# Kernel tuning notes

Hardware: AMD Instinct MI355X
Metric: run time of the kernel (lower is better)

## Reference

```python
import jax, jax.numpy as jnp
import numpy as np

B, L, D, DIN, A, V, R = 1024, 100, 256, 704, 128, 32000, 129


def setup_inputs() -> dict:
    key = jax.random.key(0)
    ks = jax.random.split(key, 18)
    s = 0.05
    inp = {
        "x": jax.random.normal(ks[0], (B, DIN), jnp.float32),
        "h0": jax.random.normal(ks[1], (B, D), jnp.float32),
        "c0": jax.random.normal(ks[2], (B, D), jnp.float32),
        "src_enc": jax.random.normal(ks[3], (B, L, D), jnp.float32),
        "src_token_ids": jax.random.randint(ks[4], (B, L), 0, V),
        "W_ih": jax.random.normal(ks[5], (4 * D, DIN), jnp.float32) * s,
        "b_ih": jax.random.normal(ks[6], (4 * D,), jnp.float32) * s,
        "W_hh": jax.random.normal(ks[7], (4 * D, D), jnp.float32) * s,
        "b_hh": jax.random.normal(ks[8], (4 * D,), jnp.float32) * s,
        "W_attn": jax.random.normal(ks[9], (D, D), jnp.float32) * s,
        "W_att_vec": jax.random.normal(ks[10], (A * 2, 2 * D), jnp.float32) * s,
        "W_ptr": jax.random.normal(ks[11], (D, D), jnp.float32) * s,
        "rule_emb": jax.random.normal(ks[12], (R, 128), jnp.float32) * s,
        "W_rule_proj": jax.random.normal(ks[13], (D, 128), jnp.float32) * s,
        "prim_emb": jax.random.normal(ks[14], (V, 128), jnp.float32) * s,
        "W_prim_proj": jax.random.normal(ks[15], (D, 128), jnp.float32) * s,
        "w_gen": jax.random.normal(ks[16], (2, D), jnp.float32) * s,
        "b_gen": jax.random.normal(ks[17], (2,), jnp.float32) * s,
    }
    # W_att_vec maps concat(h, ctx) [2D] -> ATT (=256); keep shape (256, 512)
    inp["W_att_vec"] = inp["W_att_vec"][:256]
    return inp


def reference(x, h0, c0, src_enc, src_token_ids, W_ih, b_ih, W_hh, b_hh,
              W_attn, W_att_vec, W_ptr, rule_emb, W_rule_proj,
              prim_emb, W_prim_proj, w_gen, b_gen):
    # --- LSTMCell (torch gate order i, f, g, o) ---
    gates = x @ W_ih.T + b_ih + h0 @ W_hh.T + b_hh          # [B, 4D]
    i, f, g, o = jnp.split(gates, 4, axis=-1)
    i, f, o = jax.nn.sigmoid(i), jax.nn.sigmoid(f), jax.nn.sigmoid(o)
    c = f * c0 + i * jnp.tanh(g)
    h = o * jnp.tanh(c)                                      # [B, D]

    # --- dot-product attention over source encodings ---
    enc_proj = src_enc @ W_attn.T                            # [B, L, D]
    scores = jnp.einsum('bd,bld->bl', h, enc_proj)
    alpha = jax.nn.softmax(scores, axis=-1)
    ctx = jnp.einsum('bl,bld->bd', alpha, src_enc)
    att = jnp.tanh(jnp.concatenate([h, ctx], axis=-1) @ W_att_vec.T)  # [B, 256]

    # --- apply-rule (production) readout ---
    rule_proj = rule_emb @ W_rule_proj.T                     # [R, 256]
    log_p_rule = jax.nn.log_softmax(att @ rule_proj.T, axis=-1)  # [B, R]

    # --- primitive generation readout ---
    prim_proj = prim_emb @ W_prim_proj.T                     # [V, 256]
    p_gen_prim = jax.nn.softmax(att @ prim_proj.T, axis=-1)  # [B, V]

    # --- pointer network copy distribution over source positions ---
    ptr_scores = jnp.einsum('bld,bd->bl', src_enc @ W_ptr.T, att)
    copy_p = jax.nn.softmax(ptr_scores, axis=-1)             # [B, L]

    # --- gen vs copy gate (softmax over 2, per usage in parse()) ---
    gate = jax.nn.softmax(att @ w_gen.T + b_gen, axis=-1)    # [B, 2]

    # --- combined primitive distribution: gen + scattered copy mass ---
    p_prim = gate[:, :1] * p_gen_prim                        # [B, V]
    copy_mass = gate[:, 1:] * copy_p                         # [B, L]
    bidx = jnp.arange(p_prim.shape[0])[:, None]
    p_prim = p_prim.at[bidx, src_token_ids].add(copy_mass)
    return log_p_rule, p_prim, h, c, att
```

## Files before the change

### kernel.cpp

```cpp
#include <hip/hip_runtime.h>
#include <hip/hip_bf16.h>
#include <math.h>

#define NB   1024
#define LL   100
#define DD   256
#define DINN 704
#define VV   32000
#define RR   129
#define KAV  512
#define ROWU 129

typedef float f32x4 __attribute__((ext_vector_type(4)));
typedef float f32x2 __attribute__((ext_vector_type(2)));
typedef short s16x8 __attribute__((ext_vector_type(8)));
typedef unsigned short u16;
typedef unsigned int u32;

__device__ __forceinline__ float sigf(float x) { return 1.0f / (1.0f + __expf(-x)); }

__device__ __forceinline__ u16 f2bf(float f) {
    u32 u = __float_as_uint(f);
    u += 0x7fffu + ((u >> 16) & 1u);
    return (u16)(u >> 16);
}
__device__ __forceinline__ float bf2f(u16 s) {
    return __uint_as_float(((u32)s) << 16);
}

__global__ __launch_bounds__(256) void k_conv(
    const float* __restrict__ prim_emb, u16* __restrict__ prim_bf,
    const float* __restrict__ W_ih, u16* __restrict__ wih_bf,
    const float* __restrict__ W_hh, u16* __restrict__ whh_bf,
    const float* __restrict__ x, u16* __restrict__ x_bf,
    const float* __restrict__ h0, u16* __restrict__ h0_bf,
    const float* __restrict__ rule_emb, const float* __restrict__ W_rule_proj,
    float* __restrict__ rpT)
{
    __shared__ float re_s[128];
    const int bx = blockIdx.x, t = threadIdx.x;

    const float* src; u16* dst; int off;
    if (bx < 2000)      { src = prim_emb; dst = prim_bf; off = bx * 2048; }
    else if (bx < 2352) { src = W_ih;  dst = wih_bf; off = (bx - 2000) * 2048; }
    else if (bx < 2480) { src = W_hh;  dst = whh_bf; off = (bx - 2352) * 2048; }
    else if (bx < 2832) { src = x;     dst = x_bf;   off = (bx - 2480) * 2048; }
    else                { src = h0;    dst = h0_bf;  off = (bx - 2832) * 2048; }

    if (bx < RR && t < 128) re_s[t] = rule_emb[bx * 128 + t];

    int i = off + t * 8;
    f32x4 a = *reinterpret_cast<const f32x4*>(&src[i]);
    f32x4 b = *reinterpret_cast<const f32x4*>(&src[i + 4]);
    s16x8 r;
    r[0] = (short)f2bf(a[0]); r[1] = (short)f2bf(a[1]);
    r[2] = (short)f2bf(a[2]); r[3] = (short)f2bf(a[3]);
    r[4] = (short)f2bf(b[0]); r[5] = (short)f2bf(b[1]);
    r[6] = (short)f2bf(b[2]); r[7] = (short)f2bf(b[3]);
    *reinterpret_cast<s16x8*>(&dst[i]) = r;

    if (bx < RR) {
        __syncthreads();
        float acc = 0.f;
        const float* __restrict__ wr = &W_rule_proj[t * 128];
#pragma unroll 8
        for (int k = 0; k < 128; k += 4) {
            f32x4 w4 = *reinterpret_cast<const f32x4*>(&wr[k]);
            acc += w4[0] * re_s[k] + w4[1] * re_s[k + 1]
                 + w4[2] * re_s[k + 2] + w4[3] * re_s[k + 3];
        }
        rpT[t * 192 + bx] = acc;
    }
}

__global__ __launch_bounds__(256) void k_lstm(
    const u16* __restrict__ x_bf, const u16* __restrict__ h0_bf,
    const float* __restrict__ c0,
    const u16* __restrict__ wih_bf, const u16* __restrict__ whh_bf,
    const float* __restrict__ b_ih, const float* __restrict__ b_hh,
    float* __restrict__ out_h, float* __restrict__ out_c)
{
    const int t = threadIdx.x;
    const int lane = t & 63, w = t >> 6;
    const int lm = lane & 15, lq = lane >> 4;
    const int dg = blockIdx.x;
    const int row0 = blockIdx.y * 128 + w * 32;
    f32x4 acc[4][2] = {};

    for (int kt = 0; kt < 22; ++kt) {
        const int ko = kt * 32 + lq * 8;
        s16x8 bfr[4], afr[2];
#pragma unroll
        for (int mg = 0; mg < 4; ++mg)
            bfr[mg] = *reinterpret_cast<const s16x8*>(
                &wih_bf[(mg * 256 + dg * 16 + lm) * DINN + ko]);
#pragma unroll
        for (int ng = 0; ng < 2; ++ng)
            afr[ng] = *reinterpret_cast<const s16x8*>(
                &x_bf[(row0 + ng * 16 + lm) * DINN + ko]);
#pragma unroll
        for (int mg = 0; mg < 4; ++mg)
#pragma unroll
            for (int ng = 0; ng < 2; ++ng)
                acc[mg][ng] = __builtin_amdgcn_mfma_f32_16x16x32_bf16(
                    bfr[mg], afr[ng], acc[mg][ng], 0, 0, 0);
    }
    for (int kt = 0; kt < 8; ++kt) {
        const int ko = kt * 32 + lq * 8;
        s16x8 bfr[4], afr[2];
#pragma unroll
        for (int mg = 0; mg < 4; ++mg)
            bfr[mg] = *reinterpret_cast<const s16x8*>(
                &whh_bf[(mg * 256 + dg * 16 + lm) * DD + ko]);
#pragma unroll
        for (int ng = 0; ng < 2; ++ng)
            afr[ng] = *reinterpret_cast<const s16x8*>(
                &h0_bf[(row0 + ng * 16 + lm) * DD + ko]);
#pragma unroll
        for (int mg = 0; mg < 4; ++mg)
#pragma unroll
            for (int ng = 0; ng < 2; ++ng)
                acc[mg][ng] = __builtin_amdgcn_mfma_f32_16x16x32_bf16(
                    bfr[mg], afr[ng], acc[mg][ng], 0, 0, 0);
    }

    const int dc = dg * 16 + lq * 4;
    f32x4 bi[4];
#pragma unroll
    for (int mg = 0; mg < 4; ++mg) {
        f32x4 a4 = *reinterpret_cast<const f32x4*>(&b_ih[mg * 256 + dc]);
        f32x4 b4 = *reinterpret_cast<const f32x4*>(&b_hh[mg * 256 + dc]);
        bi[mg][0] = a4[0] + b4[0]; bi[mg][1] = a4[1] + b4[1];
        bi[mg][2] = a4[2] + b4[2]; bi[mg][3] = a4[3] + b4[3];
    }
#pragma unroll
    for (int ng = 0; ng < 2; ++ng) {
        const int row = row0 + ng * 16 + lm;
        f32x4 c4 = *reinterpret_cast<const f32x4*>(&c0[row * DD + dc]);
        f32x4 h4, cc4;
#pragma unroll
        for (int r = 0; r < 4; ++r) {
            float iv = acc[0][ng][r] + bi[0][r];
            float fv = acc[1][ng][r] + bi[1][r];
            float gv = acc[2][ng][r] + bi[2][r];
            float ov = acc[3][ng][r] + bi[3][r];
            float cc = sigf(fv) * c4[r] + sigf(iv) * tanhf(gv);
            cc4[r] = cc;
            h4[r] = sigf(ov) * tanhf(cc);
        }
        *reinterpret_cast<f32x4*>(&out_c[row * DD + dc]) = cc4;
        *reinterpret_cast<f32x4*>(&out_h[row * DD + dc]) = h4;
    }
}

__global__ __launch_bounds__(256) void k_hw(
    const float* __restrict__ h, const float* __restrict__ W_attn, float* __restrict__ hW)
{
    __shared__ __align__(16) float As[16][36];
    __shared__ __align__(16) float Bs[16][68];
    const int t = threadIdx.x;
    const int row0 = blockIdx.x * 32;
    const int col0 = blockIdx.y * 64;
    const int tr = t >> 4, tc = t & 15;
    float acc[2][4] = {};
    for (int kt = 0; kt < 16; ++kt) {
        __syncthreads();
#pragma unroll
        for (int p = 0; p < 2; ++p) {
            int e = t + p * 256;
            int r = e >> 4, kk = e & 15;
            As[kk][r] = h[(row0 + r) * DD + kt * 16 + kk];
        }
#pragma unroll
        for (int p = 0; p < 4; ++p) {
            int e = t + p * 256;
            int kk = e >> 6, c = e & 63;
            Bs[kk][c] = W_attn[(kt * 16 + kk) * DD + col0 + c];
        }
        __syncthreads();
#pragma unroll
        for (int kk = 0; kk < 16; ++kk) {
            float a0 = As[kk][tr * 2], a1 = As[kk][tr * 2 + 1];
            f32x4 b = *reinterpret_cast<const f32x4*>(&Bs[kk][tc * 4]);
#pragma unroll
            for (int i = 0; i < 4; ++i) {
                acc[0][i] = fmaf(a0, b[i], acc[0][i]);
                acc[1][i] = fmaf(a1, b[i], acc[1][i]);
            }
        }
    }
#pragma unroll
    for (int j = 0; j < 2; ++j) {
        f32x4 v;
#pragma unroll
        for (int i = 0; i < 4; ++i) v[i] = acc[j][i];
        *reinterpret_cast<f32x4*>(&hW[(row0 + tr * 2 + j) * DD + col0 + tc * 4]) = v;
    }
}

__global__ __launch_bounds__(256, 2) void k_attn2(
    const float* __restrict__ src_enc, const float* __restrict__ hW,
    float* __restrict__ ctx_out)
{
    __shared__ u32 enc_u[LL * ROWU];
    __shared__ __align__(16) float part[4][DD];
    __shared__ __align__(16) float hw_s[DD];
    __shared__ float sc_s[LL];
    __shared__ float al_s[LL];

    const int b = blockIdx.x, t = threadIdx.x;
    const int lane = t & 63, w = t >> 6;
    const float* __restrict__ enc = src_enc + (size_t)b * LL * DD;

    hw_s[t] = hW[b * DD + t];

#pragma unroll
    for (int p = 0; p < 25; ++p) {
        int q = p * 256 + t;
        int l = q >> 6, dq = q & 63;
        f32x4 ev = *reinterpret_cast<const f32x4*>(&enc[l * DD + dq * 4]);
        u32 w0 = (u32)f2bf(ev[0]) | ((u32)f2bf(ev[1]) << 16);
        u32 w1 = (u32)f2bf(ev[2]) | ((u32)f2bf(ev[3]) << 16);
        enc_u[l * ROWU + dq * 2]     = w0;
        enc_u[l * ROWU + dq * 2 + 1] = w1;
    }
    __syncthreads();

    {
        const int sl = ((w >> 1) << 6) + lane;
        float sp = 0.f;
        if (sl < LL) {
            const u32* __restrict__ rp = enc_u + sl * ROWU + ((w & 1) << 6);
            const float* __restrict__ hp = hw_s + ((w & 1) << 7);
#pragma unroll 32
            for (int k = 0; k < 64; ++k) {
                u32 v = rp[k];
                sp = fmaf(bf2f((u16)v),         hp[2 * k],     sp);
                sp = fmaf(bf2f((u16)(v >> 16)), hp[2 * k + 1], sp);
            }
        }
        part[w][lane] = sp;
    }
    __syncthreads();
    if (t < LL) sc_s[t] = part[(t >> 6) << 1][t & 63] + part[((t >> 6) << 1) + 1][t & 63];
    __syncthreads();

    if (w == 0) {
        float v0 = sc_s[lane];
        float v1 = (lane + 64 < LL) ? sc_s[lane + 64] : -1e30f;
        float m = fmaxf(v0, v1);
#pragma unroll
        for (int s = 1; s < 64; s <<= 1) m = fmaxf(m, __shfl_xor(m, s));
        float e0 = __expf(v0 - m);
        float e1 = (lane + 64 < LL) ? __expf(v1 - m) : 0.f;
        float ssum = e0 + e1;
#pragma unroll
        for (int s = 1; s < 64; s <<= 1) ssum += __shfl_xor(ssum, s);
        float inv = 1.f / ssum;
        al_s[lane] = e0 * inv;
        if (lane + 64 < LL) al_s[lane + 64] = e1 * inv;
    }
    __syncthreads();

    {
        const int l0 = w * 25;
        float c0 = 0.f, c1 = 0.f, c2 = 0.f, c3 = 0.f;
#pragma unroll
        for (int li = 0; li < 25; ++li) {
            int l = l0 + li;
            float a = al_s[l];
            u32 v0 = enc_u[l * ROWU + lane * 2];
            u32 v1 = enc_u[l * ROWU + lane * 2 + 1];
            c0 = fmaf(a, bf2f((u16)v0), c0);
            c1 = fmaf(a, bf2f((u16)(v0 >> 16)), c1);
            c2 = fmaf(a, bf2f((u16)v1), c2);
            c3 = fmaf(a, bf2f((u16)(v1 >> 16)), c3);
        }
        f32x4 p; p[0] = c0; p[1] = c1; p[2] = c2; p[3] = c3;
        *reinterpret_cast<f32x4*>(&part[w][lane * 4]) = p;
    }
    __syncthreads();
    ctx_out[b * DD + t] = (part[0][t] + part[1][t]) + (part[2][t] + part[3][t]);
}

__global__ __launch_bounds__(256) void k_att(
    const float* __restrict__ h, const float* __restrict__ ctx,
    const float* __restrict__ W_att_vec, float* __restrict__ att_out)
{
    __shared__ __align__(16) float As[16][36];
    __shared__ __align__(16) float Bs[16][68];
    const int t = threadIdx.x;
    const int row0 = blockIdx.x * 32;
    const int col0 = blockIdx.y * 64;
    const int tr = t >> 4, tc = t & 15;
    float acc[2][4] = {};
    for (int kt = 0; kt < 32; ++kt) {
        const float* __restrict__ Asrc = (kt < 16) ? h : ctx;
        int kb = (kt < 16) ? kt * 16 : (kt - 16) * 16;
        int kg = kt * 16;
        __syncthreads();
#pragma unroll
        for (int p = 0; p < 2; ++p) {
            int e = t + p * 256;
            int r = e >> 4, kk = e & 15;
            As[kk][r] = Asrc[(row0 + r) * DD + kb + kk];
        }
#pragma unroll
        for (int p = 0; p < 4; ++p) {
            int e = t + p * 256;
            int r = e >> 4, kk = e & 15;
            Bs[kk][r] = W_att_vec[(col0 + r) * KAV + kg + kk];
        }
        __syncthreads();
#pragma unroll
        for (int kk = 0; kk < 16; ++kk) {
            float a0 = As[kk][tr * 2], a1 = As[kk][tr * 2 + 1];
            f32x4 b = *reinterpret_cast<const f32x4*>(&Bs[kk][tc * 4]);
#pragma unroll
            for (int i = 0; i < 4; ++i) {
                acc[0][i] = fmaf(a0, b[i], acc[0][i]);
                acc[1][i] = fmaf(a1, b[i], acc[1][i]);
            }
        }
    }
#pragma unroll
    for (int j = 0; j < 2; ++j)
#pragma unroll
        for (int i = 0; i < 4; ++i)
            att_out[(row0 + tr * 2 + j) * DD + col0 + tc * 4 + i] = tanhf(acc[j][i]);
}

__global__ __launch_bounds__(256) void k_ptrproj(
    const float* __restrict__ att, const float* __restrict__ W_ptr,
    const float* __restrict__ W_prim_proj, const float* __restrict__ rpT,
    float* __restrict__ atw, u16* __restrict__ att_bf, float* __restrict__ rl)
{
    __shared__ __align__(16) float As[16][36];
    __shared__ __align__(16) float Bs[16][68];
    const int t = threadIdx.x;
    const int row0 = blockIdx.x * 32;
    const int col0 = blockIdx.y * 64;
    const int tr = t >> 4, tc = t & 15;
    float acc[2][4] = {};
    for (int kt = 0; kt < 16; ++kt) {
        __syncthreads();
#pragma unroll
        for (int p = 0; p < 2; ++p) {
            int e = t + p * 256;
            int r = e >> 4, kk = e & 15;
            As[kk][r] = att[(row0 + r) * DD + kt * 16 + kk];
        }
#pragma unroll
        for (int p = 0; p < 4; ++p) {
            int e = t + p * 256;
            int kk = e >> 6, c = e & 63;
            float bv;
            if (col0 < 256)      bv = W_ptr[(kt * 16 + kk) * DD + col0 + c];
            else if (col0 < 384) bv = W_prim_proj[(kt * 16 + kk) * 128 + (col0 - 256) + c];
            else {
                int rc = col0 - 384 + c;
                bv = (rc < RR) ? rpT[(kt * 16 + kk) * 192 + rc] : 0.f;
            }
            Bs[kk][c] = bv;
        }
        __syncthreads();
#pragma unroll
        for (int kk = 0; kk < 16; ++kk) {
            float a0 = As[kk][tr * 2], a1 = As[kk][tr * 2 + 1];
            f32x4 b = *reinterpret_cast<const f32x4*>(&Bs[kk][tc * 4]);
#pragma unroll
            for (int i = 0; i < 4; ++i) {
                acc[0][i] = fmaf(a0, b[i], acc[0][i]);
                acc[1][i] = fmaf(a1, b[i], acc[1][i]);
            }
        }
    }
    if (col0 < 256) {
#pragma unroll
        for (int j = 0; j < 2; ++j) {
            f32x4 v;
#pragma unroll
            for (int i = 0; i < 4; ++i) v[i] = acc[j][i];
            *reinterpret_cast<f32x4*>(&atw[(row0 + tr * 2 + j) * DD + col0 + tc * 4]) = v;
        }
    } else if (col0 < 384) {
#pragma unroll
        for (int j = 0; j < 2; ++j)
#pragma unroll
            for (int i = 0; i < 4; ++i)
                att_bf[(row0 + tr * 2 + j) * 128 + (col0 - 256) + tc * 4 + i] = f2bf(acc[j][i]);
    } else {
#pragma unroll
        for (int j = 0; j < 2; ++j)
#pragma unroll
            for (int i = 0; i < 4; ++i) {
                int rc = col0 - 384 + tc * 4 + i;
                if (rc < RR) rl[(row0 + tr * 2 + j) * 132 + rc] = acc[j][i];
            }
    }
}

__global__ __launch_bounds__(256) void k_fin(
    const float* __restrict__ rl, const float* __restrict__ att,
    const float* __restrict__ w_gen, const float* __restrict__ b_gen,
    float* __restrict__ log_p_rule, float* __restrict__ gate0_ws,
    float* __restrict__ gate1_ws)
{
    const int w = threadIdx.x >> 6, lane = threadIdx.x & 63;
    const int b = blockIdx.x * 4 + w;

    float v0 = rl[b * 132 + lane];
    float v1 = rl[b * 132 + 64 + lane];
    float v2 = (lane == 0) ? rl[b * 132 + 128] : -1e30f;
    float m = fmaxf(fmaxf(v0, v1), v2);
#pragma unroll
    for (int s = 1; s < 64; s <<= 1) m = fmaxf(m, __shfl_xor(m, s));
    float ssum = __expf(v0 - m) + __expf(v1 - m) + ((lane == 0) ? __expf(v2 - m) : 0.f);
#pragma unroll
    for (int s = 1; s < 64; s <<= 1) ssum += __shfl_xor(ssum, s);
    float ls = m + logf(ssum);
    log_p_rule[b * RR + lane] = v0 - ls;
    log_p_rule[b * RR + 64 + lane] = v1 - ls;
    if (lane == 0) log_p_rule[b * RR + 128] = v2 - ls;

    f32x4 a4 = *reinterpret_cast<const f32x4*>(&att[b * DD + lane * 4]);
    f32x4 g0 = *reinterpret_cast<const f32x4*>(&w_gen[lane * 4]);
    f32x4 g1 = *reinterpret_cast<const f32x4*>(&w_gen[DD + lane * 4]);
    float p0 = a4[0] * g0[0] + a4[1] * g0[1] + a4[2] * g0[2] + a4[3] * g0[3];
    float p1 = a4[0] * g1[0] + a4[1] * g1[1] + a4[2] * g1[2] + a4[3] * g1[3];
#pragma unroll
    for (int s = 1; s < 64; s <<= 1) { p0 += __shfl_xor(p0, s); p1 += __shfl_xor(p1, s); }
    if (lane == 0) {
        float ga = p0 + b_gen[0], gb = p1 + b_gen[1];
        float gm = fmaxf(ga, gb);
        float ea = __expf(ga - gm), eb = __expf(gb - gm);
        gate0_ws[b] = ea / (ea + eb);
        gate1_ws[b] = eb / (ea + eb);
    }
}

__global__ __launch_bounds__(256) void k_ptr2(
    const float* __restrict__ src_enc, const float* __restrict__ atw,
    const float* __restrict__ gate1_ws, float* __restrict__ copy_mass)
{
    __shared__ float sc_s[LL];
    const int b = blockIdx.x, t = threadIdx.x;
    const int lane = t & 63, w = t >> 6;
    const float* __restrict__ enc = src_enc + (size_t)b * LL * DD;
    f32x4 aw4 = *reinterpret_cast<const f32x4*>(&atw[b * DD + lane * 4]);

    for (int l = w; l < LL; l += 4) {
        f32x4 ev = *reinterpret_cast<const f32x4*>(&enc[l * DD + lane * 4]);
        float pr = aw4[0] * ev[0] + aw4[1] * ev[1] + aw4[2] * ev[2] + aw4[3] * ev[3];
#pragma unroll
        for (int m = 1; m < 64; m <<= 1) pr += __shfl_xor(pr, m);
        if (lane == 0) sc_s[l] = pr;
    }
    __syncthreads();
    if (w == 0) {
        float gate1 = gate1_ws[b];
        float v0 = sc_s[lane];
        float v1 = (lane + 64 < LL) ? sc_s[lane + 64] : -1e30f;
        float m = fmaxf(v0, v1);
#pragma unroll
        for (int s = 1; s < 64; s <<= 1) m = fmaxf(m, __shfl_xor(m, s));
        float ee0 = __expf(v0 - m);
        float ee1 = (lane + 64 < LL) ? __expf(v1 - m) : 0.f;
        float ssum = ee0 + ee1;
#pragma unroll
        for (int s = 1; s < 64; s <<= 1) ssum += __shfl_xor(ssum, s);
        float inv = 1.f / ssum;
        copy_mass[b * LL + lane] = gate1 * ee0 * inv;
        if (lane + 64 < LL) copy_mass[b * LL + lane + 64] = gate1 * ee1 * inv;
    }
}

template <int PASS>
__global__ __launch_bounds__(256) void k_prim(
    const u16* __restrict__ att_bf, const u16* __restrict__ prim_bf,
    const float* __restrict__ coef, float* __restrict__ stats, float* __restrict__ p_prim)
{
    const int t = threadIdx.x;
    const int lane = t & 63, w = t >> 6;
    const int lm = lane & 15, lq = lane >> 4;
    const int colbase = blockIdx.x * 128 + (w & 1) * 64;
    const int chunk = colbase >> 6;
    const int rowblk = blockIdx.y * 256;

    s16x8 pfr[4][4];
#pragma unroll
    for (int kg = 0; kg < 4; ++kg)
#pragma unroll
        for (int mg = 0; mg < 4; ++mg)
            pfr[kg][mg] = *reinterpret_cast<const s16x8*>(
                &prim_bf[(size_t)(colbase + mg * 16 + lm) * 128 + kg * 32 + lq * 8]);

    for (int it = 0; it < 2; ++it) {
        const int rowbase = rowblk + it * 128 + (w >> 1) * 64;
        f32x4 acc[4][4] = {};
#pragma unroll
        for (int kg = 0; kg < 4; ++kg) {
            s16x8 afr[4];
#pragma unroll
            for (int ng = 0; ng < 4; ++ng)
                afr[ng] = *reinterpret_cast<const s16x8*>(
                    &att_bf[(rowbase + ng * 16 + lm) * 128 + kg * 32 + lq * 8]);
#pragma unroll
            for (int mg = 0; mg < 4; ++mg)
#pragma unroll
                for (int ng = 0; ng < 4; ++ng)
                    acc[mg][ng] = __builtin_amdgcn_mfma_f32_16x16x32_bf16(
                        pfr[kg][mg], afr[ng], acc[mg][ng], 0, 0, 0);
        }
        if (PASS == 0) {
#pragma unroll
            for (int ng = 0; ng < 4; ++ng) {
                float se = 0.f;
#pragma unroll
                for (int mg = 0; mg < 4; ++mg)
                    se += __expf(acc[mg][ng][0]) + __expf(acc[mg][ng][1])
                        + __expf(acc[mg][ng][2]) + __expf(acc[mg][ng][3]);
                se += __shfl_xor(se, 16);
                se += __shfl_xor(se, 32);
                if (lq == 0)
                    stats[chunk * NB + rowbase + ng * 16 + lm] = se;
            }
        } else {
#pragma unroll
            for (int ng = 0; ng < 4; ++ng) {
                const int arow = rowbase + ng * 16 + lm;
                const float cf = coef[arow];
                float* __restrict__ dst = &p_prim[(size_t)arow * VV + colbase + lq * 4];
#pragma unroll
                for (int mg = 0; mg < 4; ++mg) {
                    f32x4 v;
                    v[0] = cf * __expf(acc[mg][ng][0]);
                    v[1] = cf * __expf(acc[mg][ng][1]);
                    v[2] = cf * __expf(acc[mg][ng][2]);
                    v[3] = cf * __expf(acc[mg][ng][3]);
                    *reinterpret_cast<f32x4*>(&dst[mg * 16]) = v;
                }
            }
        }
    }
}

__global__ __launch_bounds__(256) void k_combine(
    const float* __restrict__ stats, const float* __restrict__ gate0_ws,
    float* __restrict__ coef)
{
    const int row = blockIdx.x * 256 + threadIdx.x;
    float s0 = 0.f, s1 = 0.f, s2 = 0.f, s3 = 0.f;
    for (int c = 0; c < 500; c += 4) {
        s0 += stats[(c)     * NB + row];
        s1 += stats[(c + 1) * NB + row];
        s2 += stats[(c + 2) * NB + row];
        s3 += stats[(c + 3) * NB + row];
    }
    coef[row] = gate0_ws[row] / ((s0 + s1) + (s2 + s3));
}

__global__ __launch_bounds__(256) void k_scatter(
    const int* __restrict__ tok, const float* __restrict__ copy_mass, float* __restrict__ p_prim)
{
    int i = blockIdx.x * 256 + threadIdx.x;
    if (i >= NB * LL) return;
    int b = i / LL;
    atomicAdd(&p_prim[(size_t)b * VV + tok[i]], copy_mass[i]);
}

extern "C" void kernel_launch(void* const* d_in, const int* in_sizes, int n_in,
                              void* d_out, int out_size, void* d_ws, size_t ws_size,
                              hipStream_t stream)
{
    const float* x         = (const float*)d_in[0];
    const float* h0        = (const float*)d_in[1];
    const float* c0        = (const float*)d_in[2];
    const float* src_enc   = (const float*)d_in[3];
    const int*   tok       = (const int*)  d_in[4];
    const float* W_ih      = (const float*)d_in[5];
    const float* b_ih      = (const float*)d_in[6];
    const float* W_hh      = (const float*)d_in[7];
    const float* b_hh      = (const float*)d_in[8];
    const float* W_attn    = (const float*)d_in[9];
    const float* W_att_vec = (const float*)d_in[10];
    const float* W_ptr     = (const float*)d_in[11];
    const float* rule_emb  = (const float*)d_in[12];
    const float* W_rule_pr = (const float*)d_in[13];
    const float* prim_emb  = (const float*)d_in[14];
    const float* W_prim_pr = (const float*)d_in[15];
    const float* w_gen     = (const float*)d_in[16];
    const float* b_gen     = (const float*)d_in[17];

    float* out    = (float*)d_out;
    float* o_logp = out;
    float* o_pp   = out + 1024 * 129;
    float* o_h    = o_pp + (size_t)1024 * 32000;
    float* o_c    = o_h + 1024 * 256;
    float* o_att  = o_c + 1024 * 256;

    float* wsf      = (float*)d_ws;
    float* ws_rpT   = wsf;
    float* ws_rl    = ws_rpT   + 49152;
    float* ws_gate0 = ws_rl    + 135168;
    float* ws_gate1 = ws_gate0 + 1024;
    float* ws_cm    = ws_gate1 + 1024;
    float* ws_coef  = ws_cm    + 102400;
    float* ws_hw    = ws_coef  + 1024;
    float* ws_ctx   = ws_hw    + 262144;
    float* ws_atw   = ws_ctx   + 262144;
    float* ws_stats = ws_atw   + 262144;
    u16*   ub       = (u16*)(ws_stats + 512000);
    u16*   ws_attbf = ub;
    u16*   ws_primbf= ws_attbf + 131072;
    u16*   ws_xb    = ws_primbf + 4096000;
    u16*   ws_h0b   = ws_xb    + 720896;
    u16*   ws_wihb  = ws_h0b   + 262144;
    u16*   ws_whhb  = ws_wihb  + 720896;

    k_conv<<<dim3(2960), 256, 0, stream>>>(prim_emb, ws_primbf, W_ih, ws_wihb,
                                           W_hh, ws_whhb, x, ws_xb, h0, ws_h0b,
                                           rule_emb, W_rule_pr, ws_rpT);
    k_lstm<<<dim3(16, 8), 256, 0, stream>>>(ws_xb, ws_h0b, c0, ws_wihb, ws_whhb,
                                            b_ih, b_hh, o_h, o_c);
    k_hw<<<dim3(32, 4), 256, 0, stream>>>(o_h, W_attn, ws_hw);
    k_attn2<<<dim3(1024), 256, 0, stream>>>(src_enc, ws_hw, ws_ctx);
    k_att<<<dim3(32, 4), 256, 0, stream>>>(o_h, ws_ctx, W_att_vec, o_att);
    k_ptrproj<<<dim3(32, 9), 256, 0, stream>>>(o_att, W_ptr, W_prim_pr, ws_rpT,
                                               ws_atw, ws_attbf, ws_rl);
    k_fin<<<dim3(256), 256, 0, stream>>>(ws_rl, o_att, w_gen, b_gen,
                                         o_logp, ws_gate0, ws_gate1);
    k_ptr2<<<dim3(1024), 256, 0, stream>>>(src_enc, ws_atw, ws_gate1, ws_cm);
    k_prim<0><<<dim3(250, 4), 256, 0, stream>>>(ws_attbf, ws_primbf, nullptr, ws_stats, nullptr);
    k_combine<<<dim3(4), 256, 0, stream>>>(ws_stats, ws_gate0, ws_coef);
    k_prim<1><<<dim3(250, 4), 256, 0, stream>>>(ws_attbf, ws_primbf, ws_coef, nullptr, o_pp);
    k_scatter<<<dim3(400), 256, 0, stream>>>(tok, ws_cm, o_pp);
}
```

Before: 235.0 us.

## Fuse conversion into LSTM, fold hW into attention, merge tail kernels

```diff
diff --git a/kernel.cpp b/kernel.cpp
--- a/kernel.cpp
+++ b/kernel.cpp
@@ -12,7 +12,6 @@
 #define ROWU 129
 
 typedef float f32x4 __attribute__((ext_vector_type(4)));
-typedef float f32x2 __attribute__((ext_vector_type(2)));
 typedef short s16x8 __attribute__((ext_vector_type(8)));
 typedef unsigned short u16;
 typedef unsigned int u32;
@@ -27,39 +26,33 @@
 __device__ __forceinline__ float bf2f(u16 s) {
     return __uint_as_float(((u32)s) << 16);
 }
-
-__global__ __launch_bounds__(256) void k_conv(
-    const float* __restrict__ prim_emb, u16* __restrict__ prim_bf,
-    const float* __restrict__ W_ih, u16* __restrict__ wih_bf,
-    const float* __restrict__ W_hh, u16* __restrict__ whh_bf,
-    const float* __restrict__ x, u16* __restrict__ x_bf,
-    const float* __restrict__ h0, u16* __restrict__ h0_bf,
-    const float* __restrict__ rule_emb, const float* __restrict__ W_rule_proj,
-    float* __restrict__ rpT)
-{
-    __shared__ float re_s[128];
-    const int bx = blockIdx.x, t = threadIdx.x;
-
-    const float* src; u16* dst; int off;
-    if (bx < 2000)      { src = prim_emb; dst = prim_bf; off = bx * 2048; }
-    else if (bx < 2352) { src = W_ih;  dst = wih_bf; off = (bx - 2000) * 2048; }
-    else if (bx < 2480) { src = W_hh;  dst = whh_bf; off = (bx - 2352) * 2048; }
-    else if (bx < 2832) { src = x;     dst = x_bf;   off = (bx - 2480) * 2048; }
-    else                { src = h0;    dst = h0_bf;  off = (bx - 2832) * 2048; }
-
-    if (bx < RR && t < 128) re_s[t] = rule_emb[bx * 128 + t];
-
-    int i = off + t * 8;
-    f32x4 a = *reinterpret_cast<const f32x4*>(&src[i]);
-    f32x4 b = *reinterpret_cast<const f32x4*>(&src[i + 4]);
+__device__ __forceinline__ s16x8 pack8(const float* __restrict__ p) {
+    f32x4 a = *reinterpret_cast<const f32x4*>(p);
+    f32x4 b = *reinterpret_cast<const f32x4*>(p + 4);
     s16x8 r;
     r[0] = (short)f2bf(a[0]); r[1] = (short)f2bf(a[1]);
     r[2] = (short)f2bf(a[2]); r[3] = (short)f2bf(a[3]);
     r[4] = (short)f2bf(b[0]); r[5] = (short)f2bf(b[1]);
     r[6] = (short)f2bf(b[2]); r[7] = (short)f2bf(b[3]);
-    *reinterpret_cast<s16x8*>(&dst[i]) = r;
-
-    if (bx < RR) {
+    return r;
+}
+
+__global__ __launch_bounds__(256) void k_head(
+    const float* __restrict__ x, const float* __restrict__ h0,
+    const float* __restrict__ c0,
+    const float* __restrict__ W_ih, const float* __restrict__ W_hh,
+    const float* __restrict__ b_ih, const float* __restrict__ b_hh,
+    float* __restrict__ out_h, float* __restrict__ out_c,
+    const float* __restrict__ prim_emb, u16* __restrict__ prim_bf,
+    const float* __restrict__ rule_emb, const float* __restrict__ W_rule_proj,
+    float* __restrict__ rpT)
+{
+    __shared__ float re_s[128];
+    const int bx = blockIdx.x, t = threadIdx.x;
+
+    if (bx >= 2128) {
+        const int r = bx - 2128;
+        if (t < 128) re_s[t] = rule_emb[r * 128 + t];
         __syncthreads();
         float acc = 0.f;
         const float* __restrict__ wr = &W_rule_proj[t * 128];
@@ -69,22 +62,19 @@
             acc += w4[0] * re_s[k] + w4[1] * re_s[k + 1]
                  + w4[2] * re_s[k + 2] + w4[3] * re_s[k + 3];
         }
-        rpT[t * 192 + bx] = acc;
-    }
-}
-
-__global__ __launch_bounds__(256) void k_lstm(
-    const u16* __restrict__ x_bf, const u16* __restrict__ h0_bf,
-    const float* __restrict__ c0,
-    const u16* __restrict__ wih_bf, const u16* __restrict__ whh_bf,
-    const float* __restrict__ b_ih, const float* __restrict__ b_hh,
-    float* __restrict__ out_h, float* __restrict__ out_c)
-{
-    const int t = threadIdx.x;
+        rpT[t * 192 + r] = acc;
+        return;
+    }
+    if (bx >= 128) {
+        int i = (bx - 128) * 2048 + t * 8;
+        *reinterpret_cast<s16x8*>(&prim_bf[i]) = pack8(&prim_emb[i]);
+        return;
+    }
+
     const int lane = t & 63, w = t >> 6;
     const int lm = lane & 15, lq = lane >> 4;
-    const int dg = blockIdx.x;
-    const int row0 = blockIdx.y * 128 + w * 32;
+    const int dg = bx & 15;
+    const int row0 = (bx >> 4) * 128 + w * 32;
     f32x4 acc[4][2] = {};
 
     for (int kt = 0; kt < 22; ++kt) {
@@ -92,12 +82,10 @@
         s16x8 bfr[4], afr[2];
 #pragma unroll
         for (int mg = 0; mg < 4; ++mg)
-            bfr[mg] = *reinterpret_cast<const s16x8*>(
-                &wih_bf[(mg * 256 + dg * 16 + lm) * DINN + ko]);
+            bfr[mg] = pack8(&W_ih[(mg * 256 + dg * 16 + lm) * DINN + ko]);
 #pragma unroll
         for (int ng = 0; ng < 2; ++ng)
-            afr[ng] = *reinterpret_cast<const s16x8*>(
-                &x_bf[(row0 + ng * 16 + lm) * DINN + ko]);
+            afr[ng] = pack8(&x[(row0 + ng * 16 + lm) * DINN + ko]);
 #pragma unroll
         for (int mg = 0; mg < 4; ++mg)
 #pragma unroll
@@ -110,12 +98,10 @@
         s16x8 bfr[4], afr[2];
 #pragma unroll
         for (int mg = 0; mg < 4; ++mg)
-            bfr[mg] = *reinterpret_cast<const s16x8*>(
-                &whh_bf[(mg * 256 + dg * 16 + lm) * DD + ko]);
+            bfr[mg] = pack8(&W_hh[(mg * 256 + dg * 16 + lm) * DD + ko]);
 #pragma unroll
         for (int ng = 0; ng < 2; ++ng)
-            afr[ng] = *reinterpret_cast<const s16x8*>(
-                &h0_bf[(row0 + ng * 16 + lm) * DD + ko]);
+            afr[ng] = pack8(&h0[(row0 + ng * 16 + lm) * DD + ko]);
 #pragma unroll
         for (int mg = 0; mg < 4; ++mg)
 #pragma unroll
@@ -153,57 +139,13 @@
     }
 }
 
-__global__ __launch_bounds__(256) void k_hw(
-    const float* __restrict__ h, const float* __restrict__ W_attn, float* __restrict__ hW)
-{
-    __shared__ __align__(16) float As[16][36];
-    __shared__ __align__(16) float Bs[16][68];
-    const int t = threadIdx.x;
-    const int row0 = blockIdx.x * 32;
-    const int col0 = blockIdx.y * 64;
-    const int tr = t >> 4, tc = t & 15;
-    float acc[2][4] = {};
-    for (int kt = 0; kt < 16; ++kt) {
-        __syncthreads();
-#pragma unroll
-        for (int p = 0; p < 2; ++p) {
-            int e = t + p * 256;
-            int r = e >> 4, kk = e & 15;
-            As[kk][r] = h[(row0 + r) * DD + kt * 16 + kk];
-        }
-#pragma unroll
-        for (int p = 0; p < 4; ++p) {
-            int e = t + p * 256;
-            int kk = e >> 6, c = e & 63;
-            Bs[kk][c] = W_attn[(kt * 16 + kk) * DD + col0 + c];
-        }
-        __syncthreads();
-#pragma unroll
-        for (int kk = 0; kk < 16; ++kk) {
-            float a0 = As[kk][tr * 2], a1 = As[kk][tr * 2 + 1];
-            f32x4 b = *reinterpret_cast<const f32x4*>(&Bs[kk][tc * 4]);
-#pragma unroll
-            for (int i = 0; i < 4; ++i) {
-                acc[0][i] = fmaf(a0, b[i], acc[0][i]);
-                acc[1][i] = fmaf(a1, b[i], acc[1][i]);
-            }
-        }
-    }
-#pragma unroll
-    for (int j = 0; j < 2; ++j) {
-        f32x4 v;
-#pragma unroll
-        for (int i = 0; i < 4; ++i) v[i] = acc[j][i];
-        *reinterpret_cast<f32x4*>(&hW[(row0 + tr * 2 + j) * DD + col0 + tc * 4]) = v;
-    }
-}
-
-__global__ __launch_bounds__(256, 2) void k_attn2(
-    const float* __restrict__ src_enc, const float* __restrict__ hW,
-    float* __restrict__ ctx_out)
+__global__ __launch_bounds__(256, 2) void k_attn2b(
+    const float* __restrict__ src_enc, const float* __restrict__ h,
+    const float* __restrict__ W_attn, float* __restrict__ ctx_out)
 {
     __shared__ u32 enc_u[LL * ROWU];
     __shared__ __align__(16) float part[4][DD];
+    __shared__ __align__(16) float h_s[DD];
     __shared__ __align__(16) float hw_s[DD];
     __shared__ float sc_s[LL];
     __shared__ float al_s[LL];
@@ -212,7 +154,7 @@
     const int lane = t & 63, w = t >> 6;
     const float* __restrict__ enc = src_enc + (size_t)b * LL * DD;
 
-    hw_s[t] = hW[b * DD + t];
+    h_s[t] = h[b * DD + t];
 
 #pragma unroll
     for (int p = 0; p < 25; ++p) {
@@ -224,6 +166,22 @@
         enc_u[l * ROWU + dq * 2]     = w0;
         enc_u[l * ROWU + dq * 2 + 1] = w1;
     }
+    __syncthreads();
+
+    {
+        f32x4 p = {0.f, 0.f, 0.f, 0.f};
+        const int e0 = w * 64;
+#pragma unroll 4
+        for (int e = e0; e < e0 + 64; ++e) {
+            float hv = h_s[e];
+            f32x4 wv = *reinterpret_cast<const f32x4*>(&W_attn[e * DD + lane * 4]);
+            p[0] = fmaf(hv, wv[0], p[0]); p[1] = fmaf(hv, wv[1], p[1]);
+            p[2] = fmaf(hv, wv[2], p[2]); p[3] = fmaf(hv, wv[3], p[3]);
+        }
+        *reinterpret_cast<f32x4*>(&part[w][lane * 4]) = p;
+    }
+    __syncthreads();
+    hw_s[t] = (part[0][t] + part[1][t]) + (part[2][t] + part[3][t]);
     __syncthreads();
 
     {
@@ -400,119 +358,117 @@
     }
 }
 
-__global__ __launch_bounds__(256) void k_fin(
+__global__ __launch_bounds__(256) void k_back(
     const float* __restrict__ rl, const float* __restrict__ att,
     const float* __restrict__ w_gen, const float* __restrict__ b_gen,
     float* __restrict__ log_p_rule, float* __restrict__ gate0_ws,
-    float* __restrict__ gate1_ws)
-{
-    const int w = threadIdx.x >> 6, lane = threadIdx.x & 63;
-    const int b = blockIdx.x * 4 + w;
-
-    float v0 = rl[b * 132 + lane];
-    float v1 = rl[b * 132 + 64 + lane];
-    float v2 = (lane == 0) ? rl[b * 132 + 128] : -1e30f;
-    float m = fmaxf(fmaxf(v0, v1), v2);
-#pragma unroll
-    for (int s = 1; s < 64; s <<= 1) m = fmaxf(m, __shfl_xor(m, s));
-    float ssum = __expf(v0 - m) + __expf(v1 - m) + ((lane == 0) ? __expf(v2 - m) : 0.f);
-#pragma unroll
-    for (int s = 1; s < 64; s <<= 1) ssum += __shfl_xor(ssum, s);
-    float ls = m + logf(ssum);
-    log_p_rule[b * RR + lane] = v0 - ls;
-    log_p_rule[b * RR + 64 + lane] = v1 - ls;
-    if (lane == 0) log_p_rule[b * RR + 128] = v2 - ls;
-
-    f32x4 a4 = *reinterpret_cast<const f32x4*>(&att[b * DD + lane * 4]);
-    f32x4 g0 = *reinterpret_cast<const f32x4*>(&w_gen[lane * 4]);
-    f32x4 g1 = *reinterpret_cast<const f32x4*>(&w_gen[DD + lane * 4]);
-    float p0 = a4[0] * g0[0] + a4[1] * g0[1] + a4[2] * g0[2] + a4[3] * g0[3];
-    float p1 = a4[0] * g1[0] + a4[1] * g1[1] + a4[2] * g1[2] + a4[3] * g1[3];
-#pragma unroll
-    for (int s = 1; s < 64; s <<= 1) { p0 += __shfl_xor(p0, s); p1 += __shfl_xor(p1, s); }
-    if (lane == 0) {
-        float ga = p0 + b_gen[0], gb = p1 + b_gen[1];
-        float gm = fmaxf(ga, gb);
-        float ea = __expf(ga - gm), eb = __expf(gb - gm);
-        gate0_ws[b] = ea / (ea + eb);
-        gate1_ws[b] = eb / (ea + eb);
-    }
-}
-
-__global__ __launch_bounds__(256) void k_ptr2(
+    float* __restrict__ gate1_ws,
     const float* __restrict__ src_enc, const float* __restrict__ atw,
-    const float* __restrict__ gate1_ws, float* __restrict__ copy_mass)
+    float* __restrict__ copy_mass,
+    const u16* __restrict__ att_bf, const u16* __restrict__ prim_bf,
+    float* __restrict__ stats)
 {
     __shared__ float sc_s[LL];
-    const int b = blockIdx.x, t = threadIdx.x;
+    const int bx = blockIdx.x, t = threadIdx.x;
     const int lane = t & 63, w = t >> 6;
-    const float* __restrict__ enc = src_enc + (size_t)b * LL * DD;
-    f32x4 aw4 = *reinterpret_cast<const f32x4*>(&atw[b * DD + lane * 4]);
-
-    for (int l = w; l < LL; l += 4) {
-        f32x4 ev = *reinterpret_cast<const f32x4*>(&enc[l * DD + lane * 4]);
-        float pr = aw4[0] * ev[0] + aw4[1] * ev[1] + aw4[2] * ev[2] + aw4[3] * ev[3];
-#pragma unroll
-        for (int m = 1; m < 64; m <<= 1) pr += __shfl_xor(pr, m);
-        if (lane == 0) sc_s[l] = pr;
-    }
-    __syncthreads();
-    if (w == 0) {
-        float gate1 = gate1_ws[b];
-        float v0 = sc_s[lane];
-        float v1 = (lane + 64 < LL) ? sc_s[lane + 64] : -1e30f;
-        float m = fmaxf(v0, v1);
+
+    if (bx < 256) {
+        const int b = bx * 4 + w;
+        float v0 = rl[b * 132 + lane];
+        float v1 = rl[b * 132 + 64 + lane];
+        float v2 = (lane == 0) ? rl[b * 132 + 128] : -1e30f;
+        float m = fmaxf(fmaxf(v0, v1), v2);
 #pragma unroll
         for (int s = 1; s < 64; s <<= 1) m = fmaxf(m, __shfl_xor(m, s));
-        float ee0 = __expf(v0 - m);
-        float ee1 = (lane + 64 < LL) ? __expf(v1 - m) : 0.f;
-        float ssum = ee0 + ee1;
+        float ssum = __expf(v0 - m) + __expf(v1 - m) + ((lane == 0) ? __expf(v2 - m) : 0.f);
 #pragma unroll
         for (int s = 1; s < 64; s <<= 1) ssum += __shfl_xor(ssum, s);
-        float inv = 1.f / ssum;
-        copy_mass[b * LL + lane] = gate1 * ee0 * inv;
-        if (lane + 64 < LL) copy_mass[b * LL + lane + 64] = gate1 * ee1 * inv;
-    }
-}
-
-template <int PASS>
-__global__ __launch_bounds__(256) void k_prim(
-    const u16* __restrict__ att_bf, const u16* __restrict__ prim_bf,
-    const float* __restrict__ coef, float* __restrict__ stats, float* __restrict__ p_prim)
-{
-    const int t = threadIdx.x;
-    const int lane = t & 63, w = t >> 6;
-    const int lm = lane & 15, lq = lane >> 4;
-    const int colbase = blockIdx.x * 128 + (w & 1) * 64;
-    const int chunk = colbase >> 6;
-    const int rowblk = blockIdx.y * 256;
-
-    s16x8 pfr[4][4];
-#pragma unroll
-    for (int kg = 0; kg < 4; ++kg)
-#pragma unroll
-        for (int mg = 0; mg < 4; ++mg)
-            pfr[kg][mg] = *reinterpret_cast<const s16x8*>(
-                &prim_bf[(size_t)(colbase + mg * 16 + lm) * 128 + kg * 32 + lq * 8]);
-
-    for (int it = 0; it < 2; ++it) {
-        const int rowbase = rowblk + it * 128 + (w >> 1) * 64;
-        f32x4 acc[4][4] = {};
-#pragma unroll
-        for (int kg = 0; kg < 4; ++kg) {
-            s16x8 afr[4];
-#pragma unroll
-            for (int ng = 0; ng < 4; ++ng)
-                afr[ng] = *reinterpret_cast<const s16x8*>(
-                    &att_bf[(rowbase + ng * 16 + lm) * 128 + kg * 32 + lq * 8]);
+        float ls = m + logf(ssum);
+        log_p_rule[b * RR + lane] = v0 - ls;
+        log_p_rule[b * RR + 64 + lane] = v1 - ls;
+        if (lane == 0) log_p_rule[b * RR + 128] = v2 - ls;
+
+        f32x4 a4 = *reinterpret_cast<const f32x4*>(&att[b * DD + lane * 4]);
+        f32x4 g0 = *reinterpret_cast<const f32x4*>(&w_gen[lane * 4]);
+        f32x4 g1 = *reinterpret_cast<const f32x4*>(&w_gen[DD + lane * 4]);
+        float p0 = a4[0] * g0[0] + a4[1] * g0[1] + a4[2] * g0[2] + a4[3] * g0[3];
+        float p1 = a4[0] * g1[0] + a4[1] * g1[1] + a4[2] * g1[2] + a4[3] * g1[3];
+#pragma unroll
+        for (int s = 1; s < 64; s <<= 1) { p0 += __shfl_xor(p0, s); p1 += __shfl_xor(p1, s); }
+        if (lane == 0) {
+            float ga = p0 + b_gen[0], gb = p1 + b_gen[1];
+            float gm = fmaxf(ga, gb);
+            float ea = __expf(ga - gm), eb = __expf(gb - gm);
+            gate0_ws[b] = ea / (ea + eb);
+            gate1_ws[b] = eb / (ea + eb);
+        }
+        return;
+    }
+
+    if (bx < 1280) {
+        const int b = bx - 256;
+        const float* __restrict__ enc = src_enc + (size_t)b * LL * DD;
+        f32x4 aw4 = *reinterpret_cast<const f32x4*>(&atw[b * DD + lane * 4]);
+
+        for (int l = w; l < LL; l += 4) {
+            f32x4 ev = *reinterpret_cast<const f32x4*>(&enc[l * DD + lane * 4]);
+            float pr = aw4[0] * ev[0] + aw4[1] * ev[1] + aw4[2] * ev[2] + aw4[3] * ev[3];
+#pragma unroll
+            for (int m = 1; m < 64; m <<= 1) pr += __shfl_xor(pr, m);
+            if (lane == 0) sc_s[l] = pr;
+        }
+        __syncthreads();
+        if (w == 0) {
+            float v0 = sc_s[lane];
+            float v1 = (lane + 64 < LL) ? sc_s[lane + 64] : -1e30f;
+            float m = fmaxf(v0, v1);
+#pragma unroll
+            for (int s = 1; s < 64; s <<= 1) m = fmaxf(m, __shfl_xor(m, s));
+            float ee0 = __expf(v0 - m);
+            float ee1 = (lane + 64 < LL) ? __expf(v1 - m) : 0.f;
+            float ssum = ee0 + ee1;
+#pragma unroll
+            for (int s = 1; s < 64; s <<= 1) ssum += __shfl_xor(ssum, s);
+            float inv = 1.f / ssum;
+            copy_mass[b * LL + lane] = ee0 * inv;
+            if (lane + 64 < LL) copy_mass[b * LL + lane + 64] = ee1 * inv;
+        }
+        return;
+    }
+
+    {
+        const int cb = bx - 1280;
+        const int colb = cb % 250, rowblk = cb / 250;
+        const int lm = lane & 15, lq = lane >> 4;
+        const int colbase = colb * 128 + (w & 1) * 64;
+        const int chunk = colbase >> 6;
+        const int rowblk_g = rowblk * 256;
+
+        s16x8 pfr[4][4];
+#pragma unroll
+        for (int kg = 0; kg < 4; ++kg)
 #pragma unroll
             for (int mg = 0; mg < 4; ++mg)
+                pfr[kg][mg] = *reinterpret_cast<const s16x8*>(
+                    &prim_bf[(size_t)(colbase + mg * 16 + lm) * 128 + kg * 32 + lq * 8]);
+
+        for (int it = 0; it < 2; ++it) {
+            const int rowbase = rowblk_g + it * 128 + (w >> 1) * 64;
+            f32x4 acc[4][4] = {};
+#pragma unroll
+            for (int kg = 0; kg < 4; ++kg) {
+                s16x8 afr[4];
 #pragma unroll
                 for (int ng = 0; ng < 4; ++ng)
-                    acc[mg][ng] = __builtin_amdgcn_mfma_f32_16x16x32_bf16(
-                        pfr[kg][mg], afr[ng], acc[mg][ng], 0, 0, 0);
-        }
-        if (PASS == 0) {
+                    afr[ng] = *reinterpret_cast<const s16x8*>(
+                        &att_bf[(rowbase + ng * 16 + lm) * 128 + kg * 32 + lq * 8]);
+#pragma unroll
+                for (int mg = 0; mg < 4; ++mg)
+#pragma unroll
+                    for (int ng = 0; ng < 4; ++ng)
+                        acc[mg][ng] = __builtin_amdgcn_mfma_f32_16x16x32_bf16(
+                            pfr[kg][mg], afr[ng], acc[mg][ng], 0, 0, 0);
+            }
 #pragma unroll
             for (int ng = 0; ng < 4; ++ng) {
                 float se = 0.f;
@@ -525,21 +481,58 @@
                 if (lq == 0)
                     stats[chunk * NB + rowbase + ng * 16 + lm] = se;
             }
-        } else {
-#pragma unroll
-            for (int ng = 0; ng < 4; ++ng) {
-                const int arow = rowbase + ng * 16 + lm;
-                const float cf = coef[arow];
-                float* __restrict__ dst = &p_prim[(size_t)arow * VV + colbase + lq * 4];
-#pragma unroll
-                for (int mg = 0; mg < 4; ++mg) {
-                    f32x4 v;
-                    v[0] = cf * __expf(acc[mg][ng][0]);
-                    v[1] = cf * __expf(acc[mg][ng][1]);
-                    v[2] = cf * __expf(acc[mg][ng][2]);
-                    v[3] = cf * __expf(acc[mg][ng][3]);
-                    *reinterpret_cast<f32x4*>(&dst[mg * 16]) = v;
-                }
+        }
+    }
+}
+
+__global__ __launch_bounds__(256) void k_prim1(
+    const u16* __restrict__ att_bf, const u16* __restrict__ prim_bf,
+    const float* __restrict__ coef, float* __restrict__ p_prim)
+{
+    const int t = threadIdx.x;
+    const int lane = t & 63, w = t >> 6;
+    const int lm = lane & 15, lq = lane >> 4;
+    const int colbase = blockIdx.x * 128 + (w & 1) * 64;
+    const int rowblk = blockIdx.y * 256;
+
+    s16x8 pfr[4][4];
+#pragma unroll
+    for (int kg = 0; kg < 4; ++kg)
+#pragma unroll
+        for (int mg = 0; mg < 4; ++mg)
+            pfr[kg][mg] = *reinterpret_cast<const s16x8*>(
+                &prim_bf[(size_t)(colbase + mg * 16 + lm) * 128 + kg * 32 + lq * 8]);
+
+    for (int it = 0; it < 2; ++it) {
+        const int rowbase = rowblk + it * 128 + (w >> 1) * 64;
+        f32x4 acc[4][4] = {};
+#pragma unroll
+        for (int kg = 0; kg < 4; ++kg) {
+            s16x8 afr[4];
+#pragma unroll
+            for (int ng = 0; ng < 4; ++ng)
+                afr[ng] = *reinterpret_cast<const s16x8*>(
+                    &att_bf[(rowbase + ng * 16 + lm) * 128 + kg * 32 + lq * 8]);
+#pragma unroll
+            for (int mg = 0; mg < 4; ++mg)
+#pragma unroll
+                for (int ng = 0; ng < 4; ++ng)
+                    acc[mg][ng] = __builtin_amdgcn_mfma_f32_16x16x32_bf16(
+                        pfr[kg][mg], afr[ng], acc[mg][ng], 0, 0, 0);
+        }
+#pragma unroll
+        for (int ng = 0; ng < 4; ++ng) {
+            const int arow = rowbase + ng * 16 + lm;
+            const float cf = coef[arow];
+            float* __restrict__ dst = &p_prim[(size_t)arow * VV + colbase + lq * 4];
+#pragma unroll
+            for (int mg = 0; mg < 4; ++mg) {
+                f32x4 v;
+                v[0] = cf * __expf(acc[mg][ng][0]);
+                v[1] = cf * __expf(acc[mg][ng][1]);
+                v[2] = cf * __expf(acc[mg][ng][2]);
+                v[3] = cf * __expf(acc[mg][ng][3]);
+                *reinterpret_cast<f32x4*>(&dst[mg * 16]) = v;
             }
         }
     }
@@ -561,12 +554,13 @@
 }
 
 __global__ __launch_bounds__(256) void k_scatter(
-    const int* __restrict__ tok, const float* __restrict__ copy_mass, float* __restrict__ p_prim)
+    const int* __restrict__ tok, const float* __restrict__ copy_mass,
+    const float* __restrict__ gate1_ws, float* __restrict__ p_prim)
 {
     int i = blockIdx.x * 256 + threadIdx.x;
     if (i >= NB * LL) return;
     int b = i / LL;
-    atomicAdd(&p_prim[(size_t)b * VV + tok[i]], copy_mass[i]);
+    atomicAdd(&p_prim[(size_t)b * VV + tok[i]], gate1_ws[b] * copy_mass[i]);
 }
 
 extern "C" void kernel_launch(void* const* d_in, const int* in_sizes, int n_in,
@@ -606,33 +600,24 @@
     float* ws_gate1 = ws_gate0 + 1024;
     float* ws_cm    = ws_gate1 + 1024;
     float* ws_coef  = ws_cm    + 102400;
-    float* ws_hw    = ws_coef  + 1024;
-    float* ws_ctx   = ws_hw    + 262144;
+    float* ws_ctx   = ws_coef  + 1024;
     float* ws_atw   = ws_ctx   + 262144;
     float* ws_stats = ws_atw   + 262144;
-    u16*   ub       = (u16*)(ws_stats + 512000);
-    u16*   ws_attbf = ub;
+    u16*   ws_attbf = (u16*)(ws_stats + 512000);
     u16*   ws_primbf= ws_attbf + 131072;
-    u16*   ws_xb    = ws_primbf + 4096000;
-    u16*   ws_h0b   = ws_xb    + 720896;
-    u16*   ws_wihb  = ws_h0b   + 262144;
-    u16*   ws_whhb  = ws_wihb  + 720896;
-
-    k_conv<<<dim3(2960), 256, 0, stream>>>(prim_emb, ws_primbf, W_ih, ws_wihb,
-                                           W_hh, ws_whhb, x, ws_xb, h0, ws_h0b,
+
+    k_head<<<dim3(2257), 256, 0, stream>>>(x, h0, c0, W_ih, W_hh, b_ih, b_hh,
+                                           o_h, o_c, prim_emb, ws_primbf,
                                            rule_emb, W_rule_pr, ws_rpT);
-    k_lstm<<<dim3(16, 8), 256, 0, stream>>>(ws_xb, ws_h0b, c0, ws_wihb, ws_whhb,
-                                            b_ih, b_hh, o_h, o_c);
-    k_hw<<<dim3(32, 4), 256, 0, stream>>>(o_h, W_attn, ws_hw);
-    k_attn2<<<dim3(1024), 256, 0, stream>>>(src_enc, ws_hw, ws_ctx);
+    k_attn2b<<<dim3(1024), 256, 0, stream>>>(src_enc, o_h, W_attn, ws_ctx);
     k_att<<<dim3(32, 4), 256, 0, stream>>>(o_h, ws_ctx, W_att_vec, o_att);
     k_ptrproj<<<dim3(32, 9), 256, 0, stream>>>(o_att, W_ptr, W_prim_pr, ws_rpT,
                                                ws_atw, ws_attbf, ws_rl);
-    k_fin<<<dim3(256), 256, 0, stream>>>(ws_rl, o_att, w_gen, b_gen,
-                                         o_logp, ws_gate0, ws_gate1);
-    k_ptr2<<<dim3(1024), 256, 0, stream>>>(src_enc, ws_atw, ws_gate1, ws_cm);
-    k_prim<0><<<dim3(250, 4), 256, 0, stream>>>(ws_attbf, ws_primbf, nullptr, ws_stats, nullptr);
+    k_back<<<dim3(2280), 256, 0, stream>>>(ws_rl, o_att, w_gen, b_gen,
+                                           o_logp, ws_gate0, ws_gate1,
+                                           src_enc, ws_atw, ws_cm,
+                                           ws_attbf, ws_primbf, ws_stats);
     k_combine<<<dim3(4), 256, 0, stream>>>(ws_stats, ws_gate0, ws_coef);
-    k_prim<1><<<dim3(250, 4), 256, 0, stream>>>(ws_attbf, ws_primbf, ws_coef, nullptr, o_pp);
-    k_scatter<<<dim3(400), 256, 0, stream>>>(tok, ws_cm, o_pp);
-}
+    k_prim1<<<dim3(250, 4), 256, 0, stream>>>(ws_attbf, ws_primbf, ws_coef, o_pp);
+    k_scatter<<<dim3(400), 256, 0, stream>>>(tok, ws_cm, ws_gate1, o_pp);
+}
```

Result: slower. 246.8 us (+5.1%).
